# Performance work log

Hardware: AMD Instinct MI355X
Metric: run time of the kernel (lower is better)

Reference implementation:

```python
import jax, jax.numpy as jnp
import numpy as np

B, T, N, CIN, H, K, HOR = 64, 12, 800, 2, 64, 3, 12
TCOV_IN, TCOV_H, MNUM, MDIM = 60, 2, 4, 8
KAPPA = 0.05
IN0 = CIN + TCOV_H  # layer-0 input dim: data channels + time-covariate embedding


def setup_inputs() -> dict:
    key = jax.random.key(0)
    ks = jax.random.split(key, 24)
    def nrm(k, shape, s=0.1):
        return jax.random.normal(k, shape, jnp.float32) * s
    inp = {}
    inp["x_seq"] = jax.random.normal(ks[0], (B, T, N, CIN), jnp.float32)
    inp["t_x"] = jax.random.normal(ks[1], (B, T, TCOV_IN), jnp.float32)
    inp["t_y"] = jax.random.normal(ks[2], (B, HOR, TCOV_IN), jnp.float32)
    # adaptive graph as in init_adp_graph: softmax(relu(v1 @ v2), axis=1)
    inp["G"] = jax.nn.softmax(jax.nn.relu(nrm(ks[3], (N, 20), 1.0) @ nrm(ks[4], (20, N), 1.0)), axis=1)
    i = 5
    for pre in ("enc", "dec"):
        for l, hin in enumerate((IN0, H)):
            inp[f"{pre}_Wg{l}"] = nrm(ks[i], ((hin + H) * K, 2 * H)); i += 1
            inp[f"{pre}_bg{l}"] = jnp.zeros((2 * H,), jnp.float32)
            inp[f"{pre}_Wc{l}"] = nrm(ks[i], ((hin + H) * K, H)); i += 1
            inp[f"{pre}_bc{l}"] = jnp.zeros((H,), jnp.float32)
    inp["mlp_W1"] = nrm(ks[i], (TCOV_IN, 10)); i += 1
    inp["mlp_b1"] = jnp.zeros((10,), jnp.float32)
    inp["mlp_W2"] = nrm(ks[i], (10, TCOV_H * N)); i += 1
    inp["mlp_b2"] = jnp.zeros((TCOV_H * N,), jnp.float32)
    inp["memory"] = nrm(ks[i], (MNUM, MDIM), 1.0); i += 1
    inp["Wa"] = nrm(ks[i], (N * H, MDIM), 0.01); i += 1
    inp["fc"] = nrm(ks[i], (MDIM, MDIM * N), 0.1); i += 1
    inp["proj_W"] = nrm(ks[i], (H + MDIM, CIN)); i += 1
    inp["proj_b"] = jnp.zeros((CIN,), jnp.float32)
    return inp


def _cheby(G):
    # Chebyshev basis T_0..T_{K-1}: T_0=I, T_1=G, T_k = 2 G T_{k-1} - T_{k-2}
    Gs = [jnp.eye(N, dtype=G.dtype), G]
    for _ in range(2, K):
        Gs.append(2.0 * (G @ Gs[-1]) - Gs[-2])
    return jnp.stack(Gs[:K])  # (K, N, N)


def _gconv(x, Gs, W, b):
    # mixhop: h_k = kappa*x + (1-kappa) * einsum('bnp,nm->bmp', x, T_k); concat over k, then project
    agg = KAPPA * x[None] + (1.0 - KAPPA) * jnp.einsum('bnp,knm->kbmp', x, Gs)  # (K,B,N,P)
    Bq, Nq, P = x.shape
    h = jnp.transpose(agg, (1, 2, 0, 3)).reshape(Bq, Nq, K * P)  # matches torch.cat order
    return h @ W + b


def _cell(x, h, Gs, Wg, bg, Wc, bc):
    # GCRU cell: graph-conv GRU
    ur = _gconv(jnp.concatenate([x, h], -1), Gs, Wg, bg)
    u, r = jnp.split(ur, 2, axis=-1)
    u = jax.nn.sigmoid(u)
    r = jax.nn.sigmoid(r)
    c = jnp.tanh(_gconv(jnp.concatenate([x, r * h], -1), Gs, Wc, bc))
    return (1.0 - u) * h + u * c


def _mlp(t, W1, b1, W2, b2):
    # nn.Sequential(Linear, Linear) -- no activation in between
    return (t @ W1 + b1) @ W2 + b2


def reference(x_seq, t_x, t_y, G, enc_Wg0, enc_bg0, enc_Wc0, enc_bc0, enc_Wg1, enc_bg1, enc_Wc1, enc_bc1, dec_Wg0, dec_bg0, dec_Wc0, dec_bc0, dec_Wg1, dec_bg1, dec_Wc1, dec_bc1, mlp_W1, mlp_b1, mlp_W2, mlp_b2, memory, Wa, fc, proj_W, proj_b):
    Gs = _cheby(G)
    # time covariates for encoder input
    tx_emb = _mlp(t_x, mlp_W1, mlp_b1, mlp_W2, mlp_b2).reshape(B, T, N, TCOV_H)
    x = jnp.concatenate([x_seq, tx_emb], -1)  # (B,T,N,IN0)
    # encoder: scan over time per layer
    seq = jnp.swapaxes(x, 0, 1)  # (T,B,N,.)
    enc_params = [(enc_Wg0, enc_bg0, enc_Wc0, enc_bc0), (enc_Wg1, enc_bg1, enc_Wc1, enc_bc1)]
    h_last = []
    for (Wg, bg, Wc, bc) in enc_params:
        def step(h, xt, Wg=Wg, bg=bg, Wc=Wc, bc=bc):
            hn = _cell(xt, h, Gs, Wg, bg, Wc, bc)
            return hn, hn
        h0 = jnp.zeros((B, N, H), x.dtype)
        hT, seq = jax.lax.scan(step, h0, seq)
        h_last.append(hT)
    dec_params = [(dec_Wg0, dec_bg0, dec_Wc0, dec_bc0), (dec_Wg1, dec_bg1, dec_Wc1, dec_bc1)]
    ty = jnp.swapaxes(t_y, 0, 1)  # (HOR,B,TCOV_IN)

    def dec_step(carry, tyt):
        go, h0, h1 = carry
        tye = _mlp(tyt, mlp_W1, mlp_b1, mlp_W2, mlp_b2).reshape(B, N, TCOV_H)
        xin = jnp.concatenate([go, tye], -1)
        h0 = _cell(xin, h0, Gs, *dec_params[0])
        h1 = _cell(h0, h1, Gs, *dec_params[1])
        # query_st_memory
        q = h1.reshape(B, N * H) @ Wa  # (B, MDIM)
        att = jax.nn.softmax(q @ memory.T, axis=1)  # (B, MNUM)
        attm = ((att @ memory) @ fc).reshape(B, N, MDIM)
        out = jax.nn.relu(jnp.concatenate([h1, attm], -1) @ proj_W + proj_b)  # (B,N,CIN)
        return (out, h0, h1), out

    go0 = jnp.zeros((B, N, CIN), x.dtype)
    _, outs = jax.lax.scan(dec_step, (go0, h_last[0], h_last[1]), ty)
    return jnp.swapaxes(outs, 0, 1)  # (B,HOR,N,CIN)
```

## Files before the change

kernel.cpp:

```cpp
#include <hip/hip_runtime.h>
#include <math.h>

typedef _Float16 f16_t;
typedef _Float16 half8 __attribute__((ext_vector_type(8)));
typedef float f32x4 __attribute__((ext_vector_type(4)));


struct Params {
  const float *x_seq, *t_x, *t_y, *G;
  const float *Wraw[8], *bia[8];
  const float *mW1, *mb1, *mW2, *mb2, *mem, *Wa, *fc, *projW, *projb;
  float* dout;
  float *h0, *h1, *txe, *tye, *hidb, *Wat;
  f16_t *T2h, *Bpk, *Y0, *Ybig, *Uh, *rh;
  f16_t* wsp[8];
};

__device__ __forceinline__ float sigm(float x) { return 1.0f / (1.0f + expf(-x)); }

__device__ __forceinline__ int xcd_swz(int orig, int nwg) {
  int q = nwg >> 3, r = nwg & 7, xcd = orig & 7, j = orig >> 3;
  return (xcd < r ? xcd * (q + 1) : r * (q + 1) + (xcd - r) * q) + j;
}

__device__ __forceinline__ void gload16(const void* g, void* l) {
  __builtin_amdgcn_global_load_lds((const __attribute__((address_space(1))) void*)g,
                                   (__attribute__((address_space(3))) void*)l, 16, 0, 0);
}


__global__ void __launch_bounds__(256) k_pre0(Params p) {
  int nt = gridDim.x * blockDim.x, id = blockIdx.x * blockDim.x + threadIdx.x;
  float4 z = {0.f, 0.f, 0.f, 0.f};
  for (int i = id; i < 64 * 64 * 200; i += nt) { ((float4*)p.h0)[i] = z; ((float4*)p.h1)[i] = z; }
  for (int w = 0; w < 8; ++w) {
    int layer = (w >> 1) & 1, cand = w & 1;
    int P = layer ? 128 : 68, NC = cand ? 64 : 128;
    const float* W = p.Wraw[w];
    f16_t* dst = p.wsp[w];
    int tot = 3 * NC * 128;
    for (int idx = id; idx < tot; idx += nt) {
      int s = idx / (NC * 128), rem = idx - s * (NC * 128);
      int c = rem >> 7, pp = rem & 127;
      float v = 0.f;
      if (pp < P) {
        if (s == 0)
          v = W[(size_t)pp * NC + c] + 0.05f * (W[(size_t)(P + pp) * NC + c] + W[(size_t)(2 * P + pp) * NC + c]);
        else
          v = 0.95f * W[(size_t)(s * P + pp) * NC + c];
      }
      dst[idx] = (f16_t)v;
    }
  }
  for (int idx = id; idx < 15360; idx += nt) {
    int half = idx / 7680, rem = idx - half * 7680;
    int r = rem / 10, j = rem - r * 10;
    const float* tin = half ? p.t_y : p.t_x;
    float a = p.mb1[j];
    for (int k = 0; k < 60; ++k) a += tin[(size_t)r * 60 + k] * p.mW1[k * 10 + j];
    p.hidb[idx] = a;
  }
  for (int idx = id; idx < 409600; idx += nt) {
    int c = idx / 6400, r2 = idx - c * 6400;
    int n = r2 >> 3, d = r2 & 7;
    p.Wat[idx] = p.Wa[((size_t)n * 64 + c) * 8 + d];
  }
}

__global__ void __launch_bounds__(256) k_pre1(Params p) {
  __shared__ float As[16 * 68];
  __shared__ float Bs[16 * 68];
  int tid = threadIdx.x, tx = tid & 15, ty = tid >> 4;
  const float* A = p.G;
  for (int tile = blockIdx.x; tile < 169; tile += gridDim.x) {
    int bx = tile % 13, by = tile / 13;
    int rowBase = by * 64, colBase = bx * 64;
    float acc[4][4] = {};
    for (int k0 = 0; k0 < 800; k0 += 16) {
      __syncthreads();
      for (int e = tid; e < 1024; e += 256) {
        int r = e >> 4, c = e & 15;
        int gr = rowBase + r;
        As[c * 68 + r] = (gr < 800) ? A[gr * 800 + k0 + c] : 0.f;
      }
      for (int e = tid; e < 1024; e += 256) {
        int r = e >> 6, c = e & 63;
        int gc = colBase + c;
        Bs[r * 68 + c] = (gc < 800) ? A[(k0 + r) * 800 + gc] : 0.f;
      }
      __syncthreads();
#pragma unroll
      for (int kk = 0; kk < 16; ++kk) {
        float4 a4 = *(const float4*)&As[kk * 68 + ty * 4];
        float4 b4 = *(const float4*)&Bs[kk * 68 + tx * 4];
        float av[4] = {a4.x, a4.y, a4.z, a4.w};
        float bv[4] = {b4.x, b4.y, b4.z, b4.w};
#pragma unroll
        for (int i = 0; i < 4; ++i)
#pragma unroll
          for (int j = 0; j < 4; ++j) acc[i][j] += av[i] * bv[j];
      }
    }
#pragma unroll
    for (int i = 0; i < 4; ++i) {
      int m = rowBase + ty * 4 + i;
      if (m >= 800) continue;
#pragma unroll
      for (int j = 0; j < 4; ++j) {
        int n = colBase + tx * 4 + j;
        if (n < 800) p.T2h[(size_t)m * 800 + n] = (f16_t)(2.f * acc[i][j] - (m == n ? 1.f : 0.f));
      }
    }
  }
  int nt = gridDim.x * blockDim.x, id = blockIdx.x * blockDim.x + threadIdx.x;
  for (int idx = id; idx < 2 * 768 * 1600; idx += nt) {
    int half = idx / (768 * 1600), rem = idx - half * (768 * 1600);
    int r = rem / 1600, o = rem - r * 1600;
    const float* hid = p.hidb + half * 7680;
    float* emb = half ? p.tye : p.txe;
    float a = p.mb2[o];
#pragma unroll
    for (int k = 0; k < 10; ++k) a += hid[r * 10 + k] * p.mW2[k * 1600 + o];
    emb[rem] = a;
  }
}

__global__ void __launch_bounds__(256) k_pre2(Params p) {
  int nt = gridDim.x * blockDim.x, id = blockIdx.x * blockDim.x + threadIdx.x;
  for (int idx = id; idx < 7 * 50 * 4096; idx += nt) {
    int nT = idx / 204800, rem = idx - nT * 204800;
    int ks = rem >> 12, i = rem & 4095;
    int kg = i >> 10, col = (i >> 3) & 127, e = i & 7;
    int k = ks * 32 + kg * 8 + e;
    int n = nT * 128 + col;
    f16_t v = (f16_t)0.f;
    if (n < 800) v = (k < 800) ? (f16_t)p.G[(size_t)k * 800 + n] : p.T2h[(size_t)(k - 800) * 800 + n];
    p.Bpk[idx] = v;
  }
}

template <int NC, int LAYER, int CAND>
__global__ void __launch_bounds__(256, 3) g_small(Params p, int widx, int dec, int t) {
  constexpr int NNT = (NC == 128) ? 4 : 2;
  constexpr int M = 64 * NC;
  __shared__ f16_t XS[128 * 136];
  unsigned* XS32 = (unsigned*)XS;
  int tid = threadIdx.x, lane = tid & 63, wid = tid >> 6;
  int lrow = lane & 15, lgrp = lane >> 4;
  int wm, wn;
  if (NC == 128) { wm = wid >> 1; wn = wid & 1; }
  else { wm = 0; wn = wid; }
  int swz = xcd_swz(blockIdx.x, gridDim.x);
  int b = swz / 7, nBase = (swz % 7) * 128;
  const f16_t* __restrict__ wb = p.wsp[widx];
  const float* emb = dec ? p.tye : p.txe;

  {
    int rp = tid >> 3, n0 = (tid & 7) * 16;
    int ng = nBase + n0;
    bool nval = ng < 800;
    for (int pass = 0; pass < 2; ++pass) {
      float v[2][16];
#pragma unroll
      for (int par = 0; par < 2; ++par) {
        int cp = pass * 64 + 2 * rp + par;
        float* vv = v[par];
        if (!nval) {
#pragma unroll
          for (int i = 0; i < 16; ++i) vv[i] = 0.f;
        } else if (LAYER == 1) {
          if (!CAND || cp < 64) {
            const float* src = (cp < 64) ? p.h0 + ((size_t)(b * 64 + cp)) * 800 + ng
                                         : p.h1 + ((size_t)(b * 64 + cp - 64)) * 800 + ng;
#pragma unroll
            for (int q = 0; q < 4; ++q) {
              float4 f = *(const float4*)(src + q * 4);
              vv[q * 4 + 0] = f.x; vv[q * 4 + 1] = f.y; vv[q * 4 + 2] = f.z; vv[q * 4 + 3] = f.w;
            }
          } else {
            const f16_t* src = p.rh + ((size_t)(b * 64 + cp - 64)) * 800 + ng;
            half8 a0 = *(const half8*)src, a1 = *(const half8*)(src + 8);
#pragma unroll
            for (int i = 0; i < 8; ++i) { vv[i] = (float)a0[i]; vv[8 + i] = (float)a1[i]; }
          }
        } else {
          if (cp >= 68) {
#pragma unroll
            for (int i = 0; i < 16; ++i) vv[i] = 0.f;
          } else if (cp >= 4) {
            if (!CAND) {
              const float* src = p.h0 + ((size_t)(b * 64 + cp - 4)) * 800 + ng;
#pragma unroll
              for (int q = 0; q < 4; ++q) {
                float4 f = *(const float4*)(src + q * 4);
                vv[q * 4 + 0] = f.x; vv[q * 4 + 1] = f.y; vv[q * 4 + 2] = f.z; vv[q * 4 + 3] = f.w;
              }
            } else {
              const f16_t* src = p.rh + ((size_t)(b * 64 + cp - 4)) * 800 + ng;
              half8 a0 = *(const half8*)src, a1 = *(const half8*)(src + 8);
#pragma unroll
              for (int i = 0; i < 8; ++i) { vv[i] = (float)a0[i]; vv[8 + i] = (float)a1[i]; }
            }
          } else if (cp >= 2) {
#pragma unroll
            for (int i = 0; i < 16; ++i)
              vv[i] = emb[(size_t)(b * 12 + t) * 1600 + (ng + i) * 2 + (cp - 2)];
          } else {
            if (dec) {
              if (t == 0) {
#pragma unroll
                for (int i = 0; i < 16; ++i) vv[i] = 0.f;
              } else {
#pragma unroll
                for (int i = 0; i < 16; ++i)
                  vv[i] = p.dout[((size_t)(b * 12 + t - 1) * 800 + ng + i) * 2 + cp];
              }
            } else {
#pragma unroll
              for (int i = 0; i < 16; ++i)
                vv[i] = p.x_seq[((size_t)(b * 12 + t) * 800 + ng + i) * 2 + cp];
            }
          }
        }
      }
#pragma unroll
      for (int i = 0; i < 16; ++i) {
        union { f16_t h[2]; unsigned u; } pk;
        pk.h[0] = (f16_t)v[0][i];
        pk.h[1] = (f16_t)v[1][i];
        XS32[(n0 + i) * 68 + pass * 32 + rp] = pk.u;
      }
    }
  }
  __syncthreads();

  for (int s = 0; s < 3; ++s) {
    f32x4 acc[4][NNT];
#pragma unroll
    for (int i = 0; i < 4; ++i)
#pragma unroll
      for (int j = 0; j < NNT; ++j) acc[i][j] = (f32x4){0.f, 0.f, 0.f, 0.f};
#pragma unroll
    for (int ks = 0; ks < 4; ++ks) {
      half8 fa[4], fx[NNT];
#pragma unroll
      for (int mf = 0; mf < 4; ++mf)
        fa[mf] = *(const half8*)(wb + ((size_t)(s * NC + wm * 64 + mf * 16 + lrow) << 7) + ks * 32 + lgrp * 8);
#pragma unroll
      for (int nt = 0; nt < NNT; ++nt)
        fx[nt] = *(const half8*)(XS + (wn * (NNT * 16) + nt * 16 + lrow) * 136 + ks * 32 + lgrp * 8);
#pragma unroll
      for (int mf = 0; mf < 4; ++mf)
#pragma unroll
        for (int nt = 0; nt < NNT; ++nt)
          acc[mf][nt] = __builtin_amdgcn_mfma_f32_16x16x32_f16(fa[mf], fx[nt], acc[mf][nt], 0, 0, 0);
    }
#pragma unroll
    for (int mf = 0; mf < 4; ++mf)
#pragma unroll
      for (int nt = 0; nt < NNT; ++nt) {
        int n = nBase + wn * (NNT * 16) + nt * 16 + lrow;
        if (n >= 800) continue;
#pragma unroll
        for (int j = 0; j < 4; ++j) {
          int c = wm * 64 + mf * 16 + lgrp * 4 + j;
          size_t r = (size_t)(b * NC + c);
          f16_t val = (f16_t)acc[mf][nt][j];
          if (s == 0) {
            p.Y0[r * 800 + n] = val;
          } else {
            int kp = (s - 1) * 800 + n;
            p.Ybig[((size_t)(kp >> 3) * M + r) * 8 + (kp & 7)] = val;
          }
        }
      }
  }
}

template <int NCR, int MODE>
__global__ void __launch_bounds__(256, 4) g_big(Params p, int widx, float* hcur) {
  const int M = 64 * NCR;
  __shared__ f16_t AS[3 * 2048];
  __shared__ f16_t BS[3 * 4096];
  int tid = threadIdx.x, lane = tid & 63, w = tid >> 6;
  int lrow = lane & 15, lgrp = lane >> 4;
  int wm = w >> 1, wn = w & 1;
  int swz = xcd_swz(blockIdx.x, gridDim.x);
  int rBase = (swz / 7) * 64;
  int nTile = swz % 7;
  const f16_t* __restrict__ Abase = p.Ybig;
  const f16_t* __restrict__ Bbase = p.Bpk + (size_t)nTile * 204800;
  const float* bias = p.bia[widx];

  auto stage = [&](int buf, int ks) {
    gload16(Abase + ((size_t)(ks * 4 + w) * M + rBase + lane) * 8, AS + buf * 2048 + w * 512);
    gload16(Bbase + (size_t)ks * 4096 + (size_t)(w * 2 + 0) * 512 + lane * 8, BS + buf * 4096 + (w * 2 + 0) * 512);
    gload16(Bbase + (size_t)ks * 4096 + (size_t)(w * 2 + 1) * 512 + lane * 8, BS + buf * 4096 + (w * 2 + 1) * 512);
  };

  f32x4 acc[2][4];
#pragma unroll
  for (int i = 0; i < 2; ++i)
#pragma unroll
    for (int j = 0; j < 4; ++j) acc[i][j] = (f32x4){0.f, 0.f, 0.f, 0.f};

  stage(0, 0);
  stage(1, 1);
  for (int ks = 0; ks < 50; ++ks) {
    if (ks == 49) {
      asm volatile("s_waitcnt vmcnt(0)" ::: "memory");
    } else {
      asm volatile("s_waitcnt vmcnt(3)" ::: "memory");
    }
    __builtin_amdgcn_s_barrier();
    __builtin_amdgcn_sched_barrier(0);
    int cur = ks % 3;
    half8 fa[2], fb[4];
#pragma unroll
    for (int mt = 0; mt < 2; ++mt)
      fa[mt] = *(const half8*)(AS + cur * 2048 + lgrp * 512 + (wm * 32 + mt * 16 + lrow) * 8);
#pragma unroll
    for (int nt = 0; nt < 4; ++nt)
      fb[nt] = *(const half8*)(BS + cur * 4096 + lgrp * 1024 + (wn * 64 + nt * 16 + lrow) * 8);
    if (ks + 2 < 50) stage((ks + 2) % 3, ks + 2);
#pragma unroll
    for (int mt = 0; mt < 2; ++mt)
#pragma unroll
      for (int nt = 0; nt < 4; ++nt)
        acc[mt][nt] = __builtin_amdgcn_mfma_f32_16x16x32_f16(fa[mt], fb[nt], acc[mt][nt], 0, 0, 0);
  }

#pragma unroll
  for (int mt = 0; mt < 2; ++mt)
#pragma unroll
    for (int nt = 0; nt < 4; ++nt) {
      int n = nTile * 128 + wn * 64 + nt * 16 + lrow;
      if (n >= 800) continue;
#pragma unroll
      for (int j = 0; j < 4; ++j) {
        int r = rBase + wm * 32 + mt * 16 + lgrp * 4 + j;
        int b = r / NCR, c = r & (NCR - 1);
        float v = acc[mt][nt][j] + (float)p.Y0[(size_t)r * 800 + n] + bias[c];
        if (MODE == 0) {
          if (c < 64) {
            p.Uh[(size_t)(b * 64 + c) * 800 + n] = (f16_t)sigm(v);
          } else {
            int jj = c - 64;
            float hv = hcur[(size_t)(b * 64 + jj) * 800 + n];
            p.rh[(size_t)(b * 64 + jj) * 800 + n] = (f16_t)(sigm(v) * hv);
          }
        } else {
          float u = (float)p.Uh[(size_t)(b * 64 + c) * 800 + n];
          float hv = hcur[(size_t)(b * 64 + c) * 800 + n];
          hcur[(size_t)(b * 64 + c) * 800 + n] = (1.f - u) * hv + u * tanhf(v);
        }
      }
    }
}


__global__ void __launch_bounds__(256) k_att(Params p, int t) {
  __shared__ float red[256][8];
  __shared__ float attv[8];
  int b = blockIdx.x, tid = threadIdx.x;
  float acc[8] = {};
  const float* hrow = p.h1 + (size_t)b * 51200;
  for (int i = tid; i < 51200; i += 256) {
    float hv = hrow[i];
    const float* wr = p.Wat + (size_t)i * 8;
#pragma unroll
    for (int j = 0; j < 8; ++j) acc[j] += hv * wr[j];
  }
#pragma unroll
  for (int j = 0; j < 8; ++j) red[tid][j] = acc[j];
  __syncthreads();
  for (int s = 128; s > 0; s >>= 1) {
    if (tid < s) {
#pragma unroll
      for (int j = 0; j < 8; ++j) red[tid][j] += red[tid + s][j];
    }
    __syncthreads();
  }
  if (tid == 0) {
    float q[8];
#pragma unroll
    for (int j = 0; j < 8; ++j) q[j] = red[0][j];
    float sco[4], mx = -1e30f;
#pragma unroll
    for (int m = 0; m < 4; ++m) {
      float s = 0.f;
#pragma unroll
      for (int d = 0; d < 8; ++d) s += q[d] * p.mem[m * 8 + d];
      sco[m] = s;
      mx = fmaxf(mx, s);
    }
    float se = 0.f;
#pragma unroll
    for (int m = 0; m < 4; ++m) { sco[m] = expf(sco[m] - mx); se += sco[m]; }
#pragma unroll
    for (int d = 0; d < 8; ++d) {
      float av = 0.f;
#pragma unroll
      for (int m = 0; m < 4; ++m) av += (sco[m] / se) * p.mem[m * 8 + d];
      attv[d] = av;
    }
  }
  __syncthreads();
  for (int n = tid; n < 800; n += 256) {
    float attm[8];
#pragma unroll
    for (int d = 0; d < 8; ++d) {
      float s = 0.f;
#pragma unroll
      for (int m = 0; m < 8; ++m) s += attv[m] * p.fc[(size_t)m * 6400 + n * 8 + d];
      attm[d] = s;
    }
    float o0 = p.projb[0], o1 = p.projb[1];
    const float* hb = p.h1 + (size_t)b * 51200 + n;
#pragma unroll 16
    for (int j = 0; j < 64; ++j) {
      float hv = hb[(size_t)j * 800];
      o0 += hv * p.projW[j * 2 + 0];
      o1 += hv * p.projW[j * 2 + 1];
    }
#pragma unroll
    for (int d = 0; d < 8; ++d) {
      o0 += attm[d] * p.projW[(64 + d) * 2 + 0];
      o1 += attm[d] * p.projW[(64 + d) * 2 + 1];
    }
    size_t base = ((size_t)(b * 12 + t) * 800 + n) * 2;
    p.dout[base + 0] = fmaxf(o0, 0.f);
    p.dout[base + 1] = fmaxf(o1, 0.f);
  }
}


extern "C" void kernel_launch(void* const* d_in, const int* in_sizes, int n_in,
                              void* d_out, int out_size, void* d_ws, size_t ws_size,
                              hipStream_t stream) {
  Params P;
  P.x_seq = (const float*)d_in[0];
  P.t_x = (const float*)d_in[1];
  P.t_y = (const float*)d_in[2];
  P.G = (const float*)d_in[3];
  P.Wraw[0] = (const float*)d_in[4];  P.bia[0] = (const float*)d_in[5];
  P.Wraw[1] = (const float*)d_in[6];  P.bia[1] = (const float*)d_in[7];
  P.Wraw[2] = (const float*)d_in[8];  P.bia[2] = (const float*)d_in[9];
  P.Wraw[3] = (const float*)d_in[10]; P.bia[3] = (const float*)d_in[11];
  P.Wraw[4] = (const float*)d_in[12]; P.bia[4] = (const float*)d_in[13];
  P.Wraw[5] = (const float*)d_in[14]; P.bia[5] = (const float*)d_in[15];
  P.Wraw[6] = (const float*)d_in[16]; P.bia[6] = (const float*)d_in[17];
  P.Wraw[7] = (const float*)d_in[18]; P.bia[7] = (const float*)d_in[19];
  P.mW1 = (const float*)d_in[20];
  P.mb1 = (const float*)d_in[21];
  P.mW2 = (const float*)d_in[22];
  P.mb2 = (const float*)d_in[23];
  P.mem = (const float*)d_in[24];
  P.Wa = (const float*)d_in[25];
  P.fc = (const float*)d_in[26];
  P.projW = (const float*)d_in[27];
  P.projb = (const float*)d_in[28];
  P.dout = (float*)d_out;

  float* ws = (float*)d_ws;
  size_t off = 0;
  auto alloc = [&](size_t nel) { float* q = ws + off; off += (nel + 3) & ~(size_t)3; return q; };
  P.T2h = (f16_t*)alloc(320000);
  P.Bpk = (f16_t*)alloc((size_t)7 * 50 * 4096 / 2);
  P.Y0 = (f16_t*)alloc((size_t)64 * 128 * 800 / 2);
  P.Ybig = (f16_t*)alloc((size_t)1600 * 8192 / 2);
  P.Uh = (f16_t*)alloc((size_t)64 * 64 * 800 / 2);
  P.rh = (f16_t*)alloc((size_t)64 * 64 * 800 / 2);
  P.h0 = alloc((size_t)64 * 64 * 800);
  P.h1 = alloc((size_t)64 * 64 * 800);
  P.txe = alloc((size_t)768 * 1600);
  P.tye = alloc((size_t)768 * 1600);
  P.hidb = alloc(15360);
  P.Wat = alloc(409600);
  for (int w = 0; w < 8; ++w) {
    int cand = w & 1;
    int NC = cand ? 64 : 128;
    P.wsp[w] = (f16_t*)alloc((size_t)3 * NC * 128 / 2);
  }

  k_pre0<<<512, 256, 0, stream>>>(P);
  k_pre1<<<512, 256, 0, stream>>>(P);
  k_pre2<<<512, 256, 0, stream>>>(P);

  auto cell = [&](int dec, int t) {
    int w0 = dec * 4;
    g_small<128, 0, 0><<<448, 256, 0, stream>>>(P, w0 + 0, dec, t);
    g_big<128, 0><<<896, 256, 0, stream>>>(P, w0 + 0, P.h0);
    g_small<64, 0, 1><<<448, 256, 0, stream>>>(P, w0 + 1, dec, t);
    g_big<64, 1><<<448, 256, 0, stream>>>(P, w0 + 1, P.h0);
    g_small<128, 1, 0><<<448, 256, 0, stream>>>(P, w0 + 2, dec, t);
    g_big<128, 0><<<896, 256, 0, stream>>>(P, w0 + 2, P.h1);
    g_small<64, 1, 1><<<448, 256, 0, stream>>>(P, w0 + 3, dec, t);
    g_big<64, 1><<<448, 256, 0, stream>>>(P, w0 + 3, P.h1);
  };

  for (int t = 0; t < 12; ++t) cell(0, t);
  for (int t = 0; t < 12; ++t) {
    cell(1, t);
    k_att<<<64, 256, 0, stream>>>(P, t);
  }
}
```

Baseline: 7.251 ms.

## Fuse candidate-side small GEMM into gate epilogue and split attention reduction

```diff
diff --git a/kernel.cpp b/kernel.cpp
--- a/kernel.cpp
+++ b/kernel.cpp
@@ -11,8 +11,8 @@
   const float *Wraw[8], *bia[8];
   const float *mW1, *mb1, *mW2, *mb2, *mem, *Wa, *fc, *projW, *projb;
   float* dout;
-  float *h0, *h1, *txe, *tye, *hidb, *Wat;
-  f16_t *T2h, *Bpk, *Y0, *Ybig, *Uh, *rh;
+  float *h0, *h1, *txe, *tye, *hidb, *partial, *Wat;
+  f16_t *T2h, *Bpk, *Y0g, *Ybg, *Y0c, *Ybc, *Uh;
   f16_t* wsp[8];
 };
 
@@ -139,17 +139,13 @@
   }
 }
 
-template <int NC, int LAYER, int CAND>
+template <int LAYER>
 __global__ void __launch_bounds__(256, 3) g_small(Params p, int widx, int dec, int t) {
-  constexpr int NNT = (NC == 128) ? 4 : 2;
-  constexpr int M = 64 * NC;
   __shared__ f16_t XS[128 * 136];
   unsigned* XS32 = (unsigned*)XS;
   int tid = threadIdx.x, lane = tid & 63, wid = tid >> 6;
   int lrow = lane & 15, lgrp = lane >> 4;
-  int wm, wn;
-  if (NC == 128) { wm = wid >> 1; wn = wid & 1; }
-  else { wm = 0; wn = wid; }
+  int wm = wid >> 1, wn = wid & 1;
   int swz = xcd_swz(blockIdx.x, gridDim.x);
   int b = swz / 7, nBase = (swz % 7) * 128;
   const f16_t* __restrict__ wb = p.wsp[widx];
@@ -169,37 +165,23 @@
 #pragma unroll
           for (int i = 0; i < 16; ++i) vv[i] = 0.f;
         } else if (LAYER == 1) {
-          if (!CAND || cp < 64) {
-            const float* src = (cp < 64) ? p.h0 + ((size_t)(b * 64 + cp)) * 800 + ng
-                                         : p.h1 + ((size_t)(b * 64 + cp - 64)) * 800 + ng;
+          const float* src = (cp < 64) ? p.h0 + ((size_t)(b * 64 + cp)) * 800 + ng
+                                       : p.h1 + ((size_t)(b * 64 + cp - 64)) * 800 + ng;
+#pragma unroll
+          for (int q = 0; q < 4; ++q) {
+            float4 f = *(const float4*)(src + q * 4);
+            vv[q * 4 + 0] = f.x; vv[q * 4 + 1] = f.y; vv[q * 4 + 2] = f.z; vv[q * 4 + 3] = f.w;
+          }
+        } else {
+          if (cp >= 68) {
+#pragma unroll
+            for (int i = 0; i < 16; ++i) vv[i] = 0.f;
+          } else if (cp >= 4) {
+            const float* src = p.h0 + ((size_t)(b * 64 + cp - 4)) * 800 + ng;
 #pragma unroll
             for (int q = 0; q < 4; ++q) {
               float4 f = *(const float4*)(src + q * 4);
               vv[q * 4 + 0] = f.x; vv[q * 4 + 1] = f.y; vv[q * 4 + 2] = f.z; vv[q * 4 + 3] = f.w;
-            }
-          } else {
-            const f16_t* src = p.rh + ((size_t)(b * 64 + cp - 64)) * 800 + ng;
-            half8 a0 = *(const half8*)src, a1 = *(const half8*)(src + 8);
-#pragma unroll
-            for (int i = 0; i < 8; ++i) { vv[i] = (float)a0[i]; vv[8 + i] = (float)a1[i]; }
-          }
-        } else {
-          if (cp >= 68) {
-#pragma unroll
-            for (int i = 0; i < 16; ++i) vv[i] = 0.f;
-          } else if (cp >= 4) {
-            if (!CAND) {
-              const float* src = p.h0 + ((size_t)(b * 64 + cp - 4)) * 800 + ng;
-#pragma unroll
-              for (int q = 0; q < 4; ++q) {
-                float4 f = *(const float4*)(src + q * 4);
-                vv[q * 4 + 0] = f.x; vv[q * 4 + 1] = f.y; vv[q * 4 + 2] = f.z; vv[q * 4 + 3] = f.w;
-              }
-            } else {
-              const f16_t* src = p.rh + ((size_t)(b * 64 + cp - 4)) * 800 + ng;
-              half8 a0 = *(const half8*)src, a1 = *(const half8*)(src + 8);
-#pragma unroll
-              for (int i = 0; i < 8; ++i) { vv[i] = (float)a0[i]; vv[8 + i] = (float)a1[i]; }
             }
           } else if (cp >= 2) {
 #pragma unroll
@@ -235,65 +217,69 @@
   __syncthreads();
 
   for (int s = 0; s < 3; ++s) {
-    f32x4 acc[4][NNT];
+    f32x4 acc[4][4];
 #pragma unroll
     for (int i = 0; i < 4; ++i)
 #pragma unroll
-      for (int j = 0; j < NNT; ++j) acc[i][j] = (f32x4){0.f, 0.f, 0.f, 0.f};
+      for (int j = 0; j < 4; ++j) acc[i][j] = (f32x4){0.f, 0.f, 0.f, 0.f};
 #pragma unroll
     for (int ks = 0; ks < 4; ++ks) {
-      half8 fa[4], fx[NNT];
+      half8 fa[4], fx[4];
 #pragma unroll
       for (int mf = 0; mf < 4; ++mf)
-        fa[mf] = *(const half8*)(wb + ((size_t)(s * NC + wm * 64 + mf * 16 + lrow) << 7) + ks * 32 + lgrp * 8);
-#pragma unroll
-      for (int nt = 0; nt < NNT; ++nt)
-        fx[nt] = *(const half8*)(XS + (wn * (NNT * 16) + nt * 16 + lrow) * 136 + ks * 32 + lgrp * 8);
+        fa[mf] = *(const half8*)(wb + ((size_t)(s * 128 + wm * 64 + mf * 16 + lrow) << 7) + ks * 32 + lgrp * 8);
+#pragma unroll
+      for (int nt = 0; nt < 4; ++nt)
+        fx[nt] = *(const half8*)(XS + (wn * 64 + nt * 16 + lrow) * 136 + ks * 32 + lgrp * 8);
 #pragma unroll
       for (int mf = 0; mf < 4; ++mf)
 #pragma unroll
-        for (int nt = 0; nt < NNT; ++nt)
+        for (int nt = 0; nt < 4; ++nt)
           acc[mf][nt] = __builtin_amdgcn_mfma_f32_16x16x32_f16(fa[mf], fx[nt], acc[mf][nt], 0, 0, 0);
     }
 #pragma unroll
     for (int mf = 0; mf < 4; ++mf)
 #pragma unroll
-      for (int nt = 0; nt < NNT; ++nt) {
-        int n = nBase + wn * (NNT * 16) + nt * 16 + lrow;
+      for (int nt = 0; nt < 4; ++nt) {
+        int n = nBase + wn * 64 + nt * 16 + lrow;
         if (n >= 800) continue;
 #pragma unroll
         for (int j = 0; j < 4; ++j) {
           int c = wm * 64 + mf * 16 + lgrp * 4 + j;
-          size_t r = (size_t)(b * NC + c);
+          size_t r = (size_t)(b * 128 + c);
           f16_t val = (f16_t)acc[mf][nt][j];
           if (s == 0) {
-            p.Y0[r * 800 + n] = val;
+            p.Y0g[r * 800 + n] = val;
           } else {
             int kp = (s - 1) * 800 + n;
-            p.Ybig[((size_t)(kp >> 3) * M + r) * 8 + (kp & 7)] = val;
+            p.Ybg[((size_t)(kp >> 3) * 8192 + r) * 8 + (kp & 7)] = val;
           }
         }
       }
   }
 }
 
-template <int NCR, int MODE>
-__global__ void __launch_bounds__(256, 4) g_big(Params p, int widx, float* hcur) {
-  const int M = 64 * NCR;
-  __shared__ f16_t AS[3 * 2048];
-  __shared__ f16_t BS[3 * 4096];
+template <int LAYER>
+__global__ void __launch_bounds__(256, 4) g_biggate(Params p, int w0, int dec, int t, float* hcur) {
+  constexpr int Pin = LAYER ? 64 : 4;
+  __shared__ __align__(16) f16_t SH[18432];
+  f16_t* AS = SH;
+  f16_t* BS = SH + 6144;
   int tid = threadIdx.x, lane = tid & 63, w = tid >> 6;
   int lrow = lane & 15, lgrp = lane >> 4;
   int wm = w >> 1, wn = w & 1;
   int swz = xcd_swz(blockIdx.x, gridDim.x);
-  int rBase = (swz / 7) * 64;
+  int rt = swz / 7;
+  int rBase = rt * 64;
   int nTile = swz % 7;
-  const f16_t* __restrict__ Abase = p.Ybig;
+  int b = rt >> 1;
+  int rhblk = rt & 1;
+  const f16_t* __restrict__ Abase = p.Ybg;
   const f16_t* __restrict__ Bbase = p.Bpk + (size_t)nTile * 204800;
-  const float* bias = p.bia[widx];
+  const float* bias = p.bia[w0];
 
   auto stage = [&](int buf, int ks) {
-    gload16(Abase + ((size_t)(ks * 4 + w) * M + rBase + lane) * 8, AS + buf * 2048 + w * 512);
+    gload16(Abase + ((size_t)(ks * 4 + w) * 8192 + rBase + lane) * 8, AS + buf * 2048 + w * 512);
     gload16(Bbase + (size_t)ks * 4096 + (size_t)(w * 2 + 0) * 512 + lane * 8, BS + buf * 4096 + (w * 2 + 0) * 512);
     gload16(Bbase + (size_t)ks * 4096 + (size_t)(w * 2 + 1) * 512 + lane * 8, BS + buf * 4096 + (w * 2 + 1) * 512);
   };
@@ -330,6 +316,195 @@
         acc[mt][nt] = __builtin_amdgcn_mfma_f32_16x16x32_f16(fa[mt], fb[nt], acc[mt][nt], 0, 0, 0);
   }
 
+  if (!rhblk) {
+#pragma unroll
+    for (int mt = 0; mt < 2; ++mt)
+#pragma unroll
+      for (int nt = 0; nt < 4; ++nt) {
+        int n = nTile * 128 + wn * 64 + nt * 16 + lrow;
+        if (n >= 800) continue;
+#pragma unroll
+        for (int j = 0; j < 4; ++j) {
+          int c = wm * 32 + mt * 16 + lgrp * 4 + j;
+          int r = rBase + c;
+          float v = acc[mt][nt][j] + (float)p.Y0g[(size_t)r * 800 + n] + bias[c];
+          p.Uh[(size_t)(b * 64 + c) * 800 + n] = (f16_t)sigm(v);
+        }
+      }
+    return;
+  }
+
+  f16_t rhv[2][4][4];
+#pragma unroll
+  for (int mt = 0; mt < 2; ++mt)
+#pragma unroll
+    for (int nt = 0; nt < 4; ++nt) {
+      int n = nTile * 128 + wn * 64 + nt * 16 + lrow;
+#pragma unroll
+      for (int j = 0; j < 4; ++j) {
+        int jj = wm * 32 + mt * 16 + lgrp * 4 + j;
+        if (n < 800) {
+          int r = rBase + jj;
+          float v = acc[mt][nt][j] + (float)p.Y0g[(size_t)r * 800 + n] + bias[64 + jj];
+          float hv = hcur[(size_t)(b * 64 + jj) * 800 + n];
+          rhv[mt][nt][j] = (f16_t)(sigm(v) * hv);
+        } else {
+          rhv[mt][nt][j] = (f16_t)0.f;
+        }
+      }
+    }
+
+  __syncthreads();
+  f16_t* Xc = SH;
+
+#pragma unroll
+  for (int mt = 0; mt < 2; ++mt)
+#pragma unroll
+    for (int nt = 0; nt < 4; ++nt) {
+      int col = wn * 64 + nt * 16 + lrow;
+#pragma unroll
+      for (int j = 0; j < 4; ++j) {
+        int jj = wm * 32 + mt * 16 + lgrp * 4 + j;
+        Xc[col * 136 + Pin + jj] = rhv[mt][nt][j];
+      }
+    }
+  if (LAYER == 1) {
+    int ct = tid >> 2, nq = tid & 3;
+    const float* src = p.h0 + (size_t)(b * 64 + ct) * 800;
+#pragma unroll 8
+    for (int i = 0; i < 32; ++i) {
+      int nl = nq * 32 + i;
+      int n = nTile * 128 + nl;
+      float v = (n < 800) ? src[n] : 0.f;
+      Xc[nl * 136 + ct] = (f16_t)v;
+    }
+  } else {
+    if (tid < 128) {
+      int col = tid;
+      int n = nTile * 128 + col;
+      float v0 = 0.f, v1 = 0.f, v2 = 0.f, v3 = 0.f;
+      if (n < 800) {
+        if (dec) {
+          if (t > 0) {
+            v0 = p.dout[((size_t)(b * 12 + t - 1) * 800 + n) * 2 + 0];
+            v1 = p.dout[((size_t)(b * 12 + t - 1) * 800 + n) * 2 + 1];
+          }
+        } else {
+          v0 = p.x_seq[((size_t)(b * 12 + t) * 800 + n) * 2 + 0];
+          v1 = p.x_seq[((size_t)(b * 12 + t) * 800 + n) * 2 + 1];
+        }
+        const float* emb = dec ? p.tye : p.txe;
+        v2 = emb[(size_t)(b * 12 + t) * 1600 + n * 2 + 0];
+        v3 = emb[(size_t)(b * 12 + t) * 1600 + n * 2 + 1];
+      }
+      Xc[col * 136 + 0] = (f16_t)v0;
+      Xc[col * 136 + 1] = (f16_t)v1;
+      Xc[col * 136 + 2] = (f16_t)v2;
+      Xc[col * 136 + 3] = (f16_t)v3;
+      unsigned* z32 = (unsigned*)(Xc + col * 136 + 68);
+#pragma unroll
+      for (int q = 0; q < 30; ++q) z32[q] = 0u;
+    }
+  }
+  __syncthreads();
+
+  const f16_t* __restrict__ wc = p.wsp[w0 + 1];
+  int cwn = w;
+  for (int s = 0; s < 3; ++s) {
+    f32x4 ac[4][2];
+#pragma unroll
+    for (int i = 0; i < 4; ++i)
+#pragma unroll
+      for (int j = 0; j < 2; ++j) ac[i][j] = (f32x4){0.f, 0.f, 0.f, 0.f};
+#pragma unroll
+    for (int ks = 0; ks < 4; ++ks) {
+      half8 fa[4], fx[2];
+#pragma unroll
+      for (int mf = 0; mf < 4; ++mf)
+        fa[mf] = *(const half8*)(wc + ((size_t)(s * 64 + mf * 16 + lrow) << 7) + ks * 32 + lgrp * 8);
+#pragma unroll
+      for (int nt = 0; nt < 2; ++nt)
+        fx[nt] = *(const half8*)(Xc + (cwn * 32 + nt * 16 + lrow) * 136 + ks * 32 + lgrp * 8);
+#pragma unroll
+      for (int mf = 0; mf < 4; ++mf)
+#pragma unroll
+        for (int nt = 0; nt < 2; ++nt)
+          ac[mf][nt] = __builtin_amdgcn_mfma_f32_16x16x32_f16(fa[mf], fx[nt], ac[mf][nt], 0, 0, 0);
+    }
+#pragma unroll
+    for (int mf = 0; mf < 4; ++mf)
+#pragma unroll
+      for (int nt = 0; nt < 2; ++nt) {
+        int n = nTile * 128 + cwn * 32 + nt * 16 + lrow;
+        if (n >= 800) continue;
+#pragma unroll
+        for (int j = 0; j < 4; ++j) {
+          int c = mf * 16 + lgrp * 4 + j;
+          size_t r = (size_t)(b * 64 + c);
+          f16_t val = (f16_t)ac[mf][nt][j];
+          if (s == 0) {
+            p.Y0c[r * 800 + n] = val;
+          } else {
+            int kp = (s - 1) * 800 + n;
+            p.Ybc[((size_t)(kp >> 3) * 4096 + r) * 8 + (kp & 7)] = val;
+          }
+        }
+      }
+  }
+}
+
+__global__ void __launch_bounds__(256, 4) g_bigcand(Params p, int widx, float* hcur) {
+  __shared__ __align__(16) f16_t SH[18432];
+  f16_t* AS = SH;
+  f16_t* BS = SH + 6144;
+  int tid = threadIdx.x, lane = tid & 63, w = tid >> 6;
+  int lrow = lane & 15, lgrp = lane >> 4;
+  int wm = w >> 1, wn = w & 1;
+  int swz = xcd_swz(blockIdx.x, gridDim.x);
+  int rBase = (swz / 7) * 64;
+  int nTile = swz % 7;
+  const f16_t* __restrict__ Abase = p.Ybc;
+  const f16_t* __restrict__ Bbase = p.Bpk + (size_t)nTile * 204800;
+  const float* bias = p.bia[widx];
+
+  auto stage = [&](int buf, int ks) {
+    gload16(Abase + ((size_t)(ks * 4 + w) * 4096 + rBase + lane) * 8, AS + buf * 2048 + w * 512);
+    gload16(Bbase + (size_t)ks * 4096 + (size_t)(w * 2 + 0) * 512 + lane * 8, BS + buf * 4096 + (w * 2 + 0) * 512);
+    gload16(Bbase + (size_t)ks * 4096 + (size_t)(w * 2 + 1) * 512 + lane * 8, BS + buf * 4096 + (w * 2 + 1) * 512);
+  };
+
+  f32x4 acc[2][4];
+#pragma unroll
+  for (int i = 0; i < 2; ++i)
+#pragma unroll
+    for (int j = 0; j < 4; ++j) acc[i][j] = (f32x4){0.f, 0.f, 0.f, 0.f};
+
+  stage(0, 0);
+  stage(1, 1);
+  for (int ks = 0; ks < 50; ++ks) {
+    if (ks == 49) {
+      asm volatile("s_waitcnt vmcnt(0)" ::: "memory");
+    } else {
+      asm volatile("s_waitcnt vmcnt(3)" ::: "memory");
+    }
+    __builtin_amdgcn_s_barrier();
+    __builtin_amdgcn_sched_barrier(0);
+    int cur = ks % 3;
+    half8 fa[2], fb[4];
+#pragma unroll
+    for (int mt = 0; mt < 2; ++mt)
+      fa[mt] = *(const half8*)(AS + cur * 2048 + lgrp * 512 + (wm * 32 + mt * 16 + lrow) * 8);
+#pragma unroll
+    for (int nt = 0; nt < 4; ++nt)
+      fb[nt] = *(const half8*)(BS + cur * 4096 + lgrp * 1024 + (wn * 64 + nt * 16 + lrow) * 8);
+    if (ks + 2 < 50) stage((ks + 2) % 3, ks + 2);
+#pragma unroll
+    for (int mt = 0; mt < 2; ++mt)
+#pragma unroll
+      for (int nt = 0; nt < 4; ++nt)
+        acc[mt][nt] = __builtin_amdgcn_mfma_f32_16x16x32_f16(fa[mt], fb[nt], acc[mt][nt], 0, 0, 0);
+  }
+
 #pragma unroll
   for (int mt = 0; mt < 2; ++mt)
 #pragma unroll
@@ -339,99 +514,96 @@
 #pragma unroll
       for (int j = 0; j < 4; ++j) {
         int r = rBase + wm * 32 + mt * 16 + lgrp * 4 + j;
-        int b = r / NCR, c = r & (NCR - 1);
-        float v = acc[mt][nt][j] + (float)p.Y0[(size_t)r * 800 + n] + bias[c];
-        if (MODE == 0) {
-          if (c < 64) {
-            p.Uh[(size_t)(b * 64 + c) * 800 + n] = (f16_t)sigm(v);
-          } else {
-            int jj = c - 64;
-            float hv = hcur[(size_t)(b * 64 + jj) * 800 + n];
-            p.rh[(size_t)(b * 64 + jj) * 800 + n] = (f16_t)(sigm(v) * hv);
-          }
-        } else {
-          float u = (float)p.Uh[(size_t)(b * 64 + c) * 800 + n];
-          float hv = hcur[(size_t)(b * 64 + c) * 800 + n];
-          hcur[(size_t)(b * 64 + c) * 800 + n] = (1.f - u) * hv + u * tanhf(v);
-        }
-      }
-    }
-}
-
-
-__global__ void __launch_bounds__(256) k_att(Params p, int t) {
-  __shared__ float red[256][8];
-  __shared__ float attv[8];
-  int b = blockIdx.x, tid = threadIdx.x;
-  float acc[8] = {};
-  const float* hrow = p.h1 + (size_t)b * 51200;
-  for (int i = tid; i < 51200; i += 256) {
-    float hv = hrow[i];
-    const float* wr = p.Wat + (size_t)i * 8;
-#pragma unroll
-    for (int j = 0; j < 8; ++j) acc[j] += hv * wr[j];
-  }
-#pragma unroll
-  for (int j = 0; j < 8; ++j) red[tid][j] = acc[j];
-  __syncthreads();
-  for (int s = 128; s > 0; s >>= 1) {
-    if (tid < s) {
-#pragma unroll
-      for (int j = 0; j < 8; ++j) red[tid][j] += red[tid + s][j];
-    }
-    __syncthreads();
-  }
-  if (tid == 0) {
-    float q[8];
-#pragma unroll
-    for (int j = 0; j < 8; ++j) q[j] = red[0][j];
-    float sco[4], mx = -1e30f;
-#pragma unroll
-    for (int m = 0; m < 4; ++m) {
-      float s = 0.f;
-#pragma unroll
-      for (int d = 0; d < 8; ++d) s += q[d] * p.mem[m * 8 + d];
-      sco[m] = s;
-      mx = fmaxf(mx, s);
-    }
-    float se = 0.f;
-#pragma unroll
-    for (int m = 0; m < 4; ++m) { sco[m] = expf(sco[m] - mx); se += sco[m]; }
-#pragma unroll
-    for (int d = 0; d < 8; ++d) {
-      float av = 0.f;
-#pragma unroll
-      for (int m = 0; m < 4; ++m) av += (sco[m] / se) * p.mem[m * 8 + d];
-      attv[d] = av;
-    }
-  }
-  __syncthreads();
-  for (int n = tid; n < 800; n += 256) {
-    float attm[8];
-#pragma unroll
-    for (int d = 0; d < 8; ++d) {
-      float s = 0.f;
-#pragma unroll
-      for (int m = 0; m < 8; ++m) s += attv[m] * p.fc[(size_t)m * 6400 + n * 8 + d];
-      attm[d] = s;
-    }
-    float o0 = p.projb[0], o1 = p.projb[1];
-    const float* hb = p.h1 + (size_t)b * 51200 + n;
+        int b = r >> 6, c = r & 63;
+        float v = acc[mt][nt][j] + (float)p.Y0c[(size_t)r * 800 + n] + bias[c];
+        float u = (float)p.Uh[(size_t)(b * 64 + c) * 800 + n];
+        float hv = hcur[(size_t)(b * 64 + c) * 800 + n];
+        hcur[(size_t)(b * 64 + c) * 800 + n] = (1.f - u) * hv + u * tanhf(v);
+      }
+    }
+}
+
+
+__global__ void __launch_bounds__(256) k_att1(Params p) {
+  int gwid = (blockIdx.x * blockDim.x + threadIdx.x) >> 6;
+  int nw = (gridDim.x * blockDim.x) >> 6;
+  int lane = threadIdx.x & 63;
+  for (int tile = gwid; tile < 1024; tile += nw) {
+    int cx = tile & 15, b = tile >> 4;
+    float acc[8] = {};
+    const float* hrow = p.h1 + (size_t)b * 51200 + cx * 3200;
+    const float* wbase = p.Wat + (size_t)cx * 3200 * 8;
+    for (int i = lane; i < 3200; i += 64) {
+      float hv = hrow[i];
+      const float* wr = wbase + (size_t)i * 8;
+#pragma unroll
+      for (int j = 0; j < 8; ++j) acc[j] += hv * wr[j];
+    }
+#pragma unroll
+    for (int s = 1; s < 64; s <<= 1) {
+#pragma unroll
+      for (int j = 0; j < 8; ++j) acc[j] += __shfl_xor(acc[j], s);
+    }
+    if (lane == 0) {
+#pragma unroll
+      for (int j = 0; j < 8; ++j) p.partial[((size_t)b * 16 + cx) * 8 + j] = acc[j];
+    }
+  }
+}
+
+__global__ void __launch_bounds__(256) k_att2(Params p, int t) {
+  int b = blockIdx.x >> 2, q4 = blockIdx.x & 3;
+  int tid = threadIdx.x;
+  float qv[8] = {};
+  for (int cx = 0; cx < 16; ++cx)
+#pragma unroll
+    for (int j = 0; j < 8; ++j) qv[j] += p.partial[((size_t)b * 16 + cx) * 8 + j];
+  float sco[4], mx = -1e30f;
+#pragma unroll
+  for (int m = 0; m < 4; ++m) {
+    float s = 0.f;
+#pragma unroll
+    for (int d = 0; d < 8; ++d) s += qv[d] * p.mem[m * 8 + d];
+    sco[m] = s;
+    mx = fmaxf(mx, s);
+  }
+  float se = 0.f;
+#pragma unroll
+  for (int m = 0; m < 4; ++m) { sco[m] = expf(sco[m] - mx); se += sco[m]; }
+  float attv[8];
+#pragma unroll
+  for (int d = 0; d < 8; ++d) {
+    float av = 0.f;
+#pragma unroll
+    for (int m = 0; m < 4; ++m) av += (sco[m] / se) * p.mem[m * 8 + d];
+    attv[d] = av;
+  }
+  if (tid >= 200) return;
+  int n = q4 * 200 + tid;
+  float attm[8];
+#pragma unroll
+  for (int d = 0; d < 8; ++d) {
+    float s = 0.f;
+#pragma unroll
+    for (int m = 0; m < 8; ++m) s += attv[m] * p.fc[(size_t)m * 6400 + n * 8 + d];
+    attm[d] = s;
+  }
+  float o0 = p.projb[0], o1 = p.projb[1];
+  const float* hb = p.h1 + (size_t)b * 51200 + n;
 #pragma unroll 16
-    for (int j = 0; j < 64; ++j) {
-      float hv = hb[(size_t)j * 800];
-      o0 += hv * p.projW[j * 2 + 0];
-      o1 += hv * p.projW[j * 2 + 1];
-    }
-#pragma unroll
-    for (int d = 0; d < 8; ++d) {
-      o0 += attm[d] * p.projW[(64 + d) * 2 + 0];
-      o1 += attm[d] * p.projW[(64 + d) * 2 + 1];
-    }
-    size_t base = ((size_t)(b * 12 + t) * 800 + n) * 2;
-    p.dout[base + 0] = fmaxf(o0, 0.f);
-    p.dout[base + 1] = fmaxf(o1, 0.f);
-  }
+  for (int j = 0; j < 64; ++j) {
+    float hv = hb[(size_t)j * 800];
+    o0 += hv * p.projW[j * 2 + 0];
+    o1 += hv * p.projW[j * 2 + 1];
+  }
+#pragma unroll
+  for (int d = 0; d < 8; ++d) {
+    o0 += attm[d] * p.projW[(64 + d) * 2 + 0];
+    o1 += attm[d] * p.projW[(64 + d) * 2 + 1];
+  }
+  size_t base = ((size_t)(b * 12 + t) * 800 + n) * 2;
+  p.dout[base + 0] = fmaxf(o0, 0.f);
+  p.dout[base + 1] = fmaxf(o1, 0.f);
 }
 
 
@@ -467,15 +639,17 @@
   auto alloc = [&](size_t nel) { float* q = ws + off; off += (nel + 3) & ~(size_t)3; return q; };
   P.T2h = (f16_t*)alloc(320000);
   P.Bpk = (f16_t*)alloc((size_t)7 * 50 * 4096 / 2);
-  P.Y0 = (f16_t*)alloc((size_t)64 * 128 * 800 / 2);
-  P.Ybig = (f16_t*)alloc((size_t)1600 * 8192 / 2);
-  P.Uh = (f16_t*)alloc((size_t)64 * 64 * 800 / 2);
-  P.rh = (f16_t*)alloc((size_t)64 * 64 * 800 / 2);
-  P.h0 = alloc((size_t)64 * 64 * 800);
-  P.h1 = alloc((size_t)64 * 64 * 800);
+  P.Y0g = (f16_t*)alloc((size_t)8192 * 800 / 2);
+  P.Ybg = (f16_t*)alloc((size_t)1600 * 8192 / 2);
+  P.Y0c = (f16_t*)alloc((size_t)4096 * 800 / 2);
+  P.Ybc = (f16_t*)alloc((size_t)1600 * 4096 / 2);
+  P.Uh = (f16_t*)alloc((size_t)4096 * 800 / 2);
+  P.h0 = alloc((size_t)4096 * 800);
+  P.h1 = alloc((size_t)4096 * 800);
   P.txe = alloc((size_t)768 * 1600);
   P.tye = alloc((size_t)768 * 1600);
   P.hidb = alloc(15360);
+  P.partial = alloc(8192);
   P.Wat = alloc(409600);
   for (int w = 0; w < 8; ++w) {
     int cand = w & 1;
@@ -489,19 +663,18 @@
 
   auto cell = [&](int dec, int t) {
     int w0 = dec * 4;
-    g_small<128, 0, 0><<<448, 256, 0, stream>>>(P, w0 + 0, dec, t);
-    g_big<128, 0><<<896, 256, 0, stream>>>(P, w0 + 0, P.h0);
-    g_small<64, 0, 1><<<448, 256, 0, stream>>>(P, w0 + 1, dec, t);
-    g_big<64, 1><<<448, 256, 0, stream>>>(P, w0 + 1, P.h0);
-    g_small<128, 1, 0><<<448, 256, 0, stream>>>(P, w0 + 2, dec, t);
-    g_big<128, 0><<<896, 256, 0, stream>>>(P, w0 + 2, P.h1);
-    g_small<64, 1, 1><<<448, 256, 0, stream>>>(P, w0 + 3, dec, t);
-    g_big<64, 1><<<448, 256, 0, stream>>>(P, w0 + 3, P.h1);
+    g_small<0><<<448, 256, 0, stream>>>(P, w0 + 0, dec, t);
+    g_biggate<0><<<896, 256, 0, stream>>>(P, w0 + 0, dec, t, P.h0);
+    g_bigcand<<<448, 256, 0, stream>>>(P, w0 + 1, P.h0);
+    g_small<1><<<448, 256, 0, stream>>>(P, w0 + 2, dec, t);
+    g_biggate<1><<<896, 256, 0, stream>>>(P, w0 + 2, dec, t, P.h1);
+    g_bigcand<<<448, 256, 0, stream>>>(P, w0 + 3, P.h1);
   };
 
   for (int t = 0; t < 12; ++t) cell(0, t);
   for (int t = 0; t < 12; ++t) {
     cell(1, t);
-    k_att<<<64, 256, 0, stream>>>(P, t);
-  }
-}
+    k_att1<<<256, 256, 0, stream>>>(P);
+    k_att2<<<256, 256, 0, stream>>>(P, t);
+  }
+}
```

After: 6.594 ms. 1.1x faster.
